# Performance work log

Measured on AMD Instinct MI355X. Metric: run time of the kernel, lower is better.

## Reference

```python
import jax, jax.numpy as jnp
import numpy as np

QMIN, QMAX = -128, 127  # get_quantized_range(8)


def setup_inputs() -> dict:
    key = jax.random.key(0)
    k1, k2, k3, k4 = jax.random.split(key, 4)
    N, IN, OUT = 8192, 4096, 4096
    x = jax.random.randint(k1, (N, IN), QMIN, QMAX + 1, dtype=jnp.int32).astype(jnp.int8)
    weight = jax.random.randint(k2, (OUT, IN), QMIN, QMAX + 1, dtype=jnp.int32).astype(jnp.int8)
    bias = jax.random.randint(k3, (OUT,), -1000, 1000, dtype=jnp.int32)
    weight_scale = jax.random.uniform(k4, (OUT,), dtype=jnp.float32, minval=1e-3, maxval=2e-2)
    return {
        "x": x,
        "weight": weight,
        "bias": bias,
        "weight_scale": weight_scale,
        "input_scale": 0.05,
        "output_scale": 0.1,
        "output_zero_point": -3,
    }


def reference(x, weight, bias, weight_scale, input_scale, output_scale, output_zero_point):
    # int8 GEMM accumulated in int32 (matches CPU path of the torch code)
    acc = jnp.matmul(x.astype(jnp.int32), weight.astype(jnp.int32).T) + bias[None, :]
    # fused per-channel dequant/requant epilogue
    scale = (input_scale * weight_scale / output_scale)[None, :]  # [1, OUT]
    out = acc.astype(jnp.float32) * scale + output_zero_point
    out = jnp.clip(jnp.round(out), QMIN, QMAX).astype(jnp.int8)
    return out
```

## Files before the change

### kernel.cpp

```cpp
#include <hip/hip_runtime.h>
#include <stdint.h>
#include <stddef.h>

typedef int v4i __attribute__((ext_vector_type(4)));

#define GLOAD16(gp, lp) __builtin_amdgcn_global_load_lds( \
    (const __attribute__((address_space(1))) void*)(gp),  \
    (__attribute__((address_space(3))) void*)(lp), 16, 0, 0)

#define PH_BAR()     __builtin_amdgcn_s_barrier()
#define WAIT_VM(n)   asm volatile("s_waitcnt vmcnt(" #n ")" ::: "memory")
#define WAIT_LGKM0() asm volatile("s_waitcnt lgkmcnt(0)" ::: "memory")
#define SCHED_FENCE() __builtin_amdgcn_sched_barrier(0)
#define PRIO1() __builtin_amdgcn_s_setprio(1)
#define PRIO0() __builtin_amdgcn_s_setprio(0)

static __device__ __forceinline__ int pack4(int a, int b, int c, int d) {
    return (a & 255) | ((b & 255) << 8) | ((c & 255) << 16) | (d << 24);
}

__global__ __launch_bounds__(256) void pack2_kernel(const int* __restrict__ srcA, v4i* __restrict__ dstA, int nA,
                                                    const int* __restrict__ srcB, v4i* __restrict__ dstB, int nB) {
    int i = blockIdx.x * blockDim.x + threadIdx.x;
    const int* src; v4i* dst;
    if (i < nA) { src = srcA; dst = dstA; }
    else { i -= nA; if (i >= nB) return; src = srcB; dst = dstB; }
    const v4i* s = reinterpret_cast<const v4i*>(src) + (size_t)i * 4;
    v4i v0 = s[0], v1 = s[1], v2 = s[2], v3 = s[3];
    v4i r;
    r.x = pack4(v0.x, v0.y, v0.z, v0.w);
    r.y = pack4(v1.x, v1.y, v1.z, v1.w);
    r.z = pack4(v2.x, v2.y, v2.z, v2.w);
    r.w = pack4(v3.x, v3.y, v3.z, v3.w);
    dst[i] = r;
}

__global__ __launch_bounds__(512, 1) void gemm_q8_mp(
    const char* __restrict__ Apk, const char* __restrict__ Bpk,
    const int* __restrict__ bias, const float* __restrict__ wscale,
    const float* __restrict__ is_p, const float* __restrict__ os_p,
    const int* __restrict__ zp_p,
    int* __restrict__ out, int K, int Ncols)
{
    __shared__ char lds[163840];

    const int tid  = threadIdx.x;
    const int wid  = tid >> 6;
    const int lane = tid & 63;
    const int l7 = lane & 7, l3 = lane >> 3;
    const int lo16 = lane & 15, hi = lane >> 4;

    int swz;
    {
        const int nwg = gridDim.x;
        const int q = nwg >> 3, r = nwg & 7;
        const int xcd = blockIdx.x & 7;
        const int base = (xcd < r) ? xcd * (q + 1) : r * (q + 1) + (xcd - r) * q;
        swz = base + (blockIdx.x >> 3);
    }
    const int nbc  = Ncols >> 8;
    const int brow = swz / nbc, bcol = swz % nbc;

    const int wr = wid >> 2, wc = wid & 3;

    const char* Ab = Apk + (size_t)(brow * 256 + wid * 8 + l3) * K + ((l7 ^ l3) << 4);
    const char* Bb = Bpk + (size_t)(bcol * 256 + wid * 8 + l3) * K + ((l7 ^ l3) << 4);

    const int colsw0 = (hi ^ l7) << 4;
    const int colsw1 = colsw0 ^ 64;
    const int aBase = (wr << 14) + (lo16 << 7);
    const int bBase = (wc << 13) + (lo16 << 7);

    v4i acc[8][4];
#pragma unroll
    for (int m = 0; m < 8; ++m)
#pragma unroll
        for (int n = 0; n < 4; ++n)
            acc[m][n] = (v4i){0, 0, 0, 0};

    v4i afA[2][2], afB[2][2], bf[4][2];

    auto stage = [&](const char* gb, int ldsOff, int h, int t) {
        const char* g = gb + (size_t)(h * 128) * K + ((size_t)t << 7);
        char* l = lds + (ldsOff + (h << 14) + (wid << 10));
        GLOAD16(g, l);
        GLOAD16(g + (size_t)64 * K, l + 8192);
    };
    auto ldAf = [&](v4i (&dst)[2][2], int bufo, int pair) {
#pragma unroll
        for (int m = 0; m < 2; ++m) {
            const int base = bufo + aBase + (pair << 12) + (m << 11);
            dst[m][0] = *(const v4i*)(lds + base + colsw0);
            dst[m][1] = *(const v4i*)(lds + base + colsw1);
        }
    };
    auto ldBf = [&](int bufo) {
#pragma unroll
        for (int n = 0; n < 4; ++n)
            bf[n][0] = *(const v4i*)(lds + 65536 + bufo + bBase + (n << 11) + colsw0);
#pragma unroll
        for (int n = 0; n < 4; ++n)
            bf[n][1] = *(const v4i*)(lds + 65536 + bufo + bBase + (n << 11) + colsw1);
    };

#define MQ(afX, p) do {                                                           \
    _Pragma("unroll") for (int s_ = 0; s_ < 2; ++s_)                              \
    _Pragma("unroll") for (int m_ = 0; m_ < 2; ++m_)                              \
    _Pragma("unroll") for (int n_ = 0; n_ < 4; ++n_)                              \
        acc[((p) << 1) + m_][n_] = __builtin_amdgcn_mfma_i32_16x16x64_i8(         \
            afX[m_][s_], bf[n_][s_], acc[((p) << 1) + m_][n_], 0, 0, 0);          \
} while (0)

    stage(Ab, 0,             0, 0);  stage(Ab, 0,             1, 0);
    stage(Bb, 65536,         0, 0);  stage(Bb, 65536,         1, 0);
    stage(Bb, 65536 + 32768, 0, 1);  stage(Bb, 65536 + 32768, 1, 1);
    WAIT_VM(4);
    PH_BAR();
    SCHED_FENCE();
    ldAf(afA, 0, 0);

    const int nt = K >> 7;
    int bcur = 0;
    for (int t = 0; t < nt - 2; ++t) {
        const int bA  = (t & 1) << 15;
        const int nbA = (~t & 1) << 15;
        int bst = bcur + 65536; if (bst >= 98304) bst -= 98304;

        ldBf(bcur);
        ldAf(afB, bA, 1);
        stage(Ab, nbA, 0, t + 1);  stage(Ab, nbA, 1, t + 1);
        PRIO1(); MQ(afA, 0); PRIO0();
        ldAf(afA, bA, 2);
        stage(Bb, 65536 + bst, 0, t + 2);  stage(Bb, 65536 + bst, 1, t + 2);
        PRIO1(); MQ(afB, 1); PRIO0();
        ldAf(afB, bA, 3);
        PRIO1(); MQ(afA, 2); PRIO0();
        WAIT_VM(4);
        WAIT_LGKM0();
        PH_BAR();
        SCHED_FENCE();
        ldAf(afA, nbA, 0);
        PRIO1(); MQ(afB, 3); PRIO0();

        bcur += 32768; if (bcur >= 98304) bcur -= 98304;
    }

    {
        const int t = nt - 2;
        const int bA  = (t & 1) << 15;
        const int nbA = (~t & 1) << 15;
        ldBf(bcur);
        ldAf(afB, bA, 1);
        stage(Ab, nbA, 0, t + 1);  stage(Ab, nbA, 1, t + 1);
        PRIO1(); MQ(afA, 0); PRIO0();
        ldAf(afA, bA, 2);
        PRIO1(); MQ(afB, 1); PRIO0();
        ldAf(afB, bA, 3);
        PRIO1(); MQ(afA, 2); PRIO0();
        WAIT_VM(0);
        WAIT_LGKM0();
        PH_BAR();
        SCHED_FENCE();
        ldAf(afA, nbA, 0);
        PRIO1(); MQ(afB, 3); PRIO0();
        bcur += 32768; if (bcur >= 98304) bcur -= 98304;
    }
    {
        const int bA = ((nt - 1) & 1) << 15;
        ldBf(bcur);
        ldAf(afB, bA, 1);
        PRIO1(); MQ(afA, 0); PRIO0();
        ldAf(afA, bA, 2);
        PRIO1(); MQ(afB, 1); PRIO0();
        ldAf(afB, bA, 3);
        PRIO1(); MQ(afA, 2); PRIO0();
        PRIO1(); MQ(afB, 3); PRIO0();
    }
#undef MQ

    const float is = *is_p, os = *os_p;
    const float zp = (float)(*zp_p);
    const int colb = (bcol << 8) + (wc << 6) + lo16;
    float sc[4]; int bv[4];
#pragma unroll
    for (int n = 0; n < 4; ++n) {
        sc[n] = is * wscale[colb + (n << 4)] / os;
        bv[n] = bias[colb + (n << 4)];
    }
#pragma unroll
    for (int m = 0; m < 8; ++m) {
#pragma unroll
        for (int j = 0; j < 4; ++j) {
            const int row = (brow << 8) + (wr << 7) + (m << 4) + (hi << 2) + j;
            int* op = out + (size_t)row * Ncols + colb;
#pragma unroll
            for (int n = 0; n < 4; ++n) {
                float f = (float)(acc[m][n][j] + bv[n]) * sc[n] + zp;
                f = rintf(f);
                f = fminf(fmaxf(f, -128.f), 127.f);
                op[n << 4] = (int)f;
            }
        }
    }
}

template <bool PACKED>
__global__ __launch_bounds__(256) void gemm_q8(
    const void* __restrict__ Ain, const void* __restrict__ Bin,
    const int* __restrict__ bias, const float* __restrict__ wscale,
    const float* __restrict__ is_p, const float* __restrict__ os_p,
    const int* __restrict__ zp_p,
    int* __restrict__ out, int Nrows, int K, int Ncols)
{
    __shared__ char Al[128 * 64];
    __shared__ char Bl[128 * 64];

    const int tid  = threadIdx.x;
    const int wid  = tid >> 6;
    const int lane = tid & 63;

    const int nbc = Ncols / 128;
    int swz = blockIdx.x;
    if ((gridDim.x & 7) == 0) {
        const int cpx = gridDim.x >> 3;
        swz = (blockIdx.x & 7) * cpx + (blockIdx.x >> 3);
    }
    const int brow = swz / nbc;
    const int bcol = swz % nbc;
    const int wr = wid >> 1, wc = wid & 1;

    v4i acc[4][4];
#pragma unroll
    for (int m = 0; m < 4; ++m)
#pragma unroll
        for (int n = 0; n < 4; ++n)
            acc[m][n] = (v4i){0, 0, 0, 0};

    const char* Ag = nullptr;
    const char* Bg = nullptr;
    if (PACKED) {
        Ag = (const char*)Ain + (size_t)(brow * 128 + wid * 32 + (lane >> 2)) * K + (lane & 3) * 16;
        Bg = (const char*)Bin + (size_t)(bcol * 128 + wid * 32 + (lane >> 2)) * K + (lane & 3) * 16;
    }
    char* aldst = Al + wid * 2048;
    char* bldst = Bl + wid * 2048;

    const int lo16 = lane & 15, hi = lane >> 4;
    const int aoff0 = (wr * 64 + lo16) * 64 + hi * 16;
    const int boff0 = (wc * 64 + lo16) * 64 + hi * 16;

    for (int k0 = 0; k0 < K; k0 += 64) {
        if (PACKED) {
            GLOAD16(Ag + k0,          aldst);
            GLOAD16(Ag + 16 * K + k0, aldst + 1024);
            GLOAD16(Bg + k0,          bldst);
            GLOAD16(Bg + 16 * K + k0, bldst + 1024);
        } else {
            const int row = tid >> 1, half = tid & 1;
            const int* sA = (const int*)Ain + (size_t)(brow * 128 + row) * K + k0 + half * 32;
            const int* sB = (const int*)Bin + (size_t)(bcol * 128 + row) * K + k0 + half * 32;
            int pa[8], pb[8];
#pragma unroll
            for (int j = 0; j < 8; ++j) {
                v4i va = reinterpret_cast<const v4i*>(sA)[j];
                v4i vb = reinterpret_cast<const v4i*>(sB)[j];
                pa[j] = pack4(va.x, va.y, va.z, va.w);
                pb[j] = pack4(vb.x, vb.y, vb.z, vb.w);
            }
            v4i* da = (v4i*)&Al[row * 64 + half * 32];
            da[0] = (v4i){pa[0], pa[1], pa[2], pa[3]};
            da[1] = (v4i){pa[4], pa[5], pa[6], pa[7]};
            v4i* db = (v4i*)&Bl[row * 64 + half * 32];
            db[0] = (v4i){pb[0], pb[1], pb[2], pb[3]};
            db[1] = (v4i){pb[4], pb[5], pb[6], pb[7]};
        }
        __syncthreads();

        v4i afr[4], bfr[4];
#pragma unroll
        for (int m = 0; m < 4; ++m)
            afr[m] = *(const v4i*)&Al[aoff0 + m * 16 * 64];
#pragma unroll
        for (int n = 0; n < 4; ++n)
            bfr[n] = *(const v4i*)&Bl[boff0 + n * 16 * 64];
#pragma unroll
        for (int m = 0; m < 4; ++m)
#pragma unroll
            for (int n = 0; n < 4; ++n)
                acc[m][n] = __builtin_amdgcn_mfma_i32_16x16x64_i8(afr[m], bfr[n], acc[m][n], 0, 0, 0);

        __syncthreads();
    }

    const float is = *is_p;
    const float os = *os_p;
    const float zp = (float)(*zp_p);
#pragma unroll
    for (int n = 0; n < 4; ++n) {
        const int col = bcol * 128 + wc * 64 + n * 16 + lo16;
        const float sc = is * wscale[col] / os;
        const int   bv = bias[col];
#pragma unroll
        for (int m = 0; m < 4; ++m) {
            const int row0 = brow * 128 + wr * 64 + m * 16 + hi * 4;
#pragma unroll
            for (int j = 0; j < 4; ++j) {
                float f = (float)(acc[m][n][j] + bv) * sc + zp;
                f = rintf(f);
                f = fminf(fmaxf(f, -128.f), 127.f);
                out[(size_t)(row0 + j) * Ncols + col] = (int)f;
            }
        }
    }
}

extern "C" void kernel_launch(void* const* d_in, const int* in_sizes, int n_in,
                              void* d_out, int out_size, void* d_ws, size_t ws_size,
                              hipStream_t stream) {
    const int*   x32    = (const int*)d_in[0];
    const int*   w32    = (const int*)d_in[1];
    const int*   bias   = (const int*)d_in[2];
    const float* wscale = (const float*)d_in[3];
    const float* isp    = (const float*)d_in[4];
    const float* osp    = (const float*)d_in[5];
    const int*   zpp    = (const int*)d_in[6];
    int* out = (int*)d_out;

    const int OUT = in_sizes[2];
    const int K   = in_sizes[1] / OUT;
    const int Nr  = in_sizes[0] / K;

    const size_t need = (size_t)Nr * K + (size_t)OUT * K;

    if (ws_size >= need) {
        char* xpk = (char*)d_ws;
        char* wpk = xpk + (size_t)Nr * K;
        const int nx16 = (Nr * K) / 16;
        const int nw16 = (OUT * K) / 16;
        pack2_kernel<<<(nx16 + nw16 + 255) / 256, 256, 0, stream>>>(
            x32, (v4i*)xpk, nx16, w32, (v4i*)wpk, nw16);
        if ((Nr & 255) == 0 && (OUT & 255) == 0 && (K & 127) == 0 && (K >> 7) >= 3) {
            const int grid8 = (Nr / 256) * (OUT / 256);
            gemm_q8_mp<<<grid8, 512, 0, stream>>>(xpk, wpk, bias, wscale, isp, osp, zpp,
                                                  out, K, OUT);
        } else {
            const int grid = (Nr / 128) * (OUT / 128);
            gemm_q8<true><<<grid, 256, 0, stream>>>(xpk, wpk, bias, wscale, isp, osp, zpp,
                                                    out, Nr, K, OUT);
        }
    } else {
        const int grid = (Nr / 128) * (OUT / 128);
        gemm_q8<false><<<grid, 256, 0, stream>>>(x32, w32, bias, wscale, isp, osp, zpp,
                                                 out, Nr, K, OUT);
    }
}
```

Baseline: 169.8 us.

## Split MFMA main loop into finer k-half phases to interleave LDS reads

Restructures the inner loop so each 128-wide k tile is processed as two 64-wide k halves. A and B fragments are loaded in smaller pieces (2 A vectors and half of B per phase) and interleaved between 8-MFMA groups, and the global-to-LDS stage calls are spread across more phases. The first B half of the next tile is prefetched after the barrier. The goal is to cut fragment register pressure and hide LDS latency better behind MFMAs. The cost is more A fragment reloads from LDS, since each A pair is now read twice per tile, and more scheduling points.

Result: no change. 172.0 us (+1.3%).

```diff
diff --git a/kernel.cpp b/kernel.cpp
--- a/kernel.cpp
+++ b/kernel.cpp
@@ -78,7 +78,7 @@
         for (int n = 0; n < 4; ++n)
             acc[m][n] = (v4i){0, 0, 0, 0};
 
-    v4i afA[2][2], afB[2][2], bf[4][2];
+    v4i afA[2], afB[2], bf[4][2];
 
     auto stage = [&](const char* gb, int ldsOff, int h, int t) {
         const char* g = gb + (size_t)(h * 128) * K + ((size_t)t << 7);
@@ -86,29 +86,23 @@
         GLOAD16(g, l);
         GLOAD16(g + (size_t)64 * K, l + 8192);
     };
-    auto ldAf = [&](v4i (&dst)[2][2], int bufo, int pair) {
-#pragma unroll
-        for (int m = 0; m < 2; ++m) {
-            const int base = bufo + aBase + (pair << 12) + (m << 11);
-            dst[m][0] = *(const v4i*)(lds + base + colsw0);
-            dst[m][1] = *(const v4i*)(lds + base + colsw1);
-        }
+    auto ldAf2 = [&](v4i (&dst)[2], int bufo, int pair, int csw) {
+#pragma unroll
+        for (int m = 0; m < 2; ++m)
+            dst[m] = *(const v4i*)(lds + bufo + aBase + (pair << 12) + (m << 11) + csw);
     };
-    auto ldBf = [&](int bufo) {
-#pragma unroll
-        for (int n = 0; n < 4; ++n)
-            bf[n][0] = *(const v4i*)(lds + 65536 + bufo + bBase + (n << 11) + colsw0);
-#pragma unroll
-        for (int n = 0; n < 4; ++n)
-            bf[n][1] = *(const v4i*)(lds + 65536 + bufo + bBase + (n << 11) + colsw1);
+    auto ldBfH = [&](int bufo, int nh, int s, int csw) {
+#pragma unroll
+        for (int k = 0; k < 2; ++k)
+            bf[(nh << 1) + k][s] =
+                *(const v4i*)(lds + 65536 + bufo + bBase + ((((nh << 1) + k)) << 11) + csw);
     };
 
-#define MQ(afX, p) do {                                                           \
-    _Pragma("unroll") for (int s_ = 0; s_ < 2; ++s_)                              \
+#define MQ8(afX, p, s) do {                                                       \
     _Pragma("unroll") for (int m_ = 0; m_ < 2; ++m_)                              \
     _Pragma("unroll") for (int n_ = 0; n_ < 4; ++n_)                              \
         acc[((p) << 1) + m_][n_] = __builtin_amdgcn_mfma_i32_16x16x64_i8(         \
-            afX[m_][s_], bf[n_][s_], acc[((p) << 1) + m_][n_], 0, 0, 0);          \
+            afX[m_], bf[n_][(s)], acc[((p) << 1) + m_][n_], 0, 0, 0);             \
 } while (0)
 
     stage(Ab, 0,             0, 0);  stage(Ab, 0,             1, 0);
@@ -117,66 +111,102 @@
     WAIT_VM(4);
     PH_BAR();
     SCHED_FENCE();
-    ldAf(afA, 0, 0);
+    ldBfH(0, 0, 0, colsw0);  ldBfH(0, 1, 0, colsw0);
+    ldAf2(afA, 0, 0, colsw0);
 
     const int nt = K >> 7;
     int bcur = 0;
     for (int t = 0; t < nt - 2; ++t) {
         const int bA  = (t & 1) << 15;
         const int nbA = (~t & 1) << 15;
-        int bst = bcur + 65536; if (bst >= 98304) bst -= 98304;
-
-        ldBf(bcur);
-        ldAf(afB, bA, 1);
-        stage(Ab, nbA, 0, t + 1);  stage(Ab, nbA, 1, t + 1);
-        PRIO1(); MQ(afA, 0); PRIO0();
-        ldAf(afA, bA, 2);
-        stage(Bb, 65536 + bst, 0, t + 2);  stage(Bb, 65536 + bst, 1, t + 2);
-        PRIO1(); MQ(afB, 1); PRIO0();
-        ldAf(afB, bA, 3);
-        PRIO1(); MQ(afA, 2); PRIO0();
+        int bnx = bcur + 32768; if (bnx >= 98304) bnx -= 98304;
+        int bst = bnx  + 32768; if (bst >= 98304) bst -= 98304;
+
+        ldAf2(afB, bA, 1, colsw0);
+        ldBfH(bcur, 0, 1, colsw1);
+        stage(Ab, nbA, 0, t + 1);
+        PRIO1(); MQ8(afA, 0, 0); PRIO0();
+        ldAf2(afA, bA, 2, colsw0);
+        ldBfH(bcur, 1, 1, colsw1);
+        stage(Ab, nbA, 1, t + 1);
+        PRIO1(); MQ8(afB, 1, 0); PRIO0();
+        ldAf2(afB, bA, 3, colsw0);
+        stage(Bb, 65536 + bst, 0, t + 2);
+        PRIO1(); MQ8(afA, 2, 0); PRIO0();
+        ldAf2(afA, bA, 0, colsw1);
+        stage(Bb, 65536 + bst, 1, t + 2);
+        PRIO1(); MQ8(afB, 3, 0); PRIO0();
+        ldAf2(afB, bA, 1, colsw1);
+        PRIO1(); MQ8(afA, 0, 1); PRIO0();
+        ldAf2(afA, bA, 2, colsw1);
+        PRIO1(); MQ8(afB, 1, 1); PRIO0();
+        ldAf2(afB, bA, 3, colsw1);
+        PRIO1(); MQ8(afA, 2, 1); PRIO0();
         WAIT_VM(4);
         WAIT_LGKM0();
         PH_BAR();
         SCHED_FENCE();
-        ldAf(afA, nbA, 0);
-        PRIO1(); MQ(afB, 3); PRIO0();
-
-        bcur += 32768; if (bcur >= 98304) bcur -= 98304;
+        ldBfH(bnx, 0, 0, colsw0);  ldBfH(bnx, 1, 0, colsw0);
+        ldAf2(afA, nbA, 0, colsw0);
+        PRIO1(); MQ8(afB, 3, 1); PRIO0();
+
+        bcur = bnx;
     }
 
     {
         const int t = nt - 2;
         const int bA  = (t & 1) << 15;
         const int nbA = (~t & 1) << 15;
-        ldBf(bcur);
-        ldAf(afB, bA, 1);
-        stage(Ab, nbA, 0, t + 1);  stage(Ab, nbA, 1, t + 1);
-        PRIO1(); MQ(afA, 0); PRIO0();
-        ldAf(afA, bA, 2);
-        PRIO1(); MQ(afB, 1); PRIO0();
-        ldAf(afB, bA, 3);
-        PRIO1(); MQ(afA, 2); PRIO0();
+        int bnx = bcur + 32768; if (bnx >= 98304) bnx -= 98304;
+
+        ldAf2(afB, bA, 1, colsw0);
+        ldBfH(bcur, 0, 1, colsw1);
+        stage(Ab, nbA, 0, t + 1);
+        PRIO1(); MQ8(afA, 0, 0); PRIO0();
+        ldAf2(afA, bA, 2, colsw0);
+        ldBfH(bcur, 1, 1, colsw1);
+        stage(Ab, nbA, 1, t + 1);
+        PRIO1(); MQ8(afB, 1, 0); PRIO0();
+        ldAf2(afB, bA, 3, colsw0);
+        PRIO1(); MQ8(afA, 2, 0); PRIO0();
+        ldAf2(afA, bA, 0, colsw1);
+        PRIO1(); MQ8(afB, 3, 0); PRIO0();
+        ldAf2(afB, bA, 1, colsw1);
+        PRIO1(); MQ8(afA, 0, 1); PRIO0();
+        ldAf2(afA, bA, 2, colsw1);
+        PRIO1(); MQ8(afB, 1, 1); PRIO0();
+        ldAf2(afB, bA, 3, colsw1);
+        PRIO1(); MQ8(afA, 2, 1); PRIO0();
         WAIT_VM(0);
         WAIT_LGKM0();
         PH_BAR();
         SCHED_FENCE();
-        ldAf(afA, nbA, 0);
-        PRIO1(); MQ(afB, 3); PRIO0();
-        bcur += 32768; if (bcur >= 98304) bcur -= 98304;
+        ldBfH(bnx, 0, 0, colsw0);  ldBfH(bnx, 1, 0, colsw0);
+        ldAf2(afA, nbA, 0, colsw0);
+        PRIO1(); MQ8(afB, 3, 1); PRIO0();
+        bcur = bnx;
     }
     {
         const int bA = ((nt - 1) & 1) << 15;
-        ldBf(bcur);
-        ldAf(afB, bA, 1);
-        PRIO1(); MQ(afA, 0); PRIO0();
-        ldAf(afA, bA, 2);
-        PRIO1(); MQ(afB, 1); PRIO0();
-        ldAf(afB, bA, 3);
-        PRIO1(); MQ(afA, 2); PRIO0();
-        PRIO1(); MQ(afB, 3); PRIO0();
-    }
-#undef MQ
+        ldAf2(afB, bA, 1, colsw0);
+        ldBfH(bcur, 0, 1, colsw1);
+        PRIO1(); MQ8(afA, 0, 0); PRIO0();
+        ldAf2(afA, bA, 2, colsw0);
+        ldBfH(bcur, 1, 1, colsw1);
+        PRIO1(); MQ8(afB, 1, 0); PRIO0();
+        ldAf2(afB, bA, 3, colsw0);
+        PRIO1(); MQ8(afA, 2, 0); PRIO0();
+        ldAf2(afA, bA, 0, colsw1);
+        PRIO1(); MQ8(afB, 3, 0); PRIO0();
+        ldAf2(afB, bA, 1, colsw1);
+        PRIO1(); MQ8(afA, 0, 1); PRIO0();
+        ldAf2(afA, bA, 2, colsw1);
+        PRIO1(); MQ8(afB, 1, 1); PRIO0();
+        ldAf2(afB, bA, 3, colsw1);
+        PRIO1(); MQ8(afA, 2, 1); PRIO0();
+        PRIO1(); MQ8(afB, 3, 1); PRIO0();
+    }
+#undef MQ8
 
     const float is = *is_p, os = *os_p;
     const float zp = (float)(*zp_p);
```

## Switch int8 GEMM main loop from 16x16x64 to 32x32x32 MFMA tiles

Applied to the files above, without the earlier changes.

Replaces the 16x16x64 int8 MFMA inner kernel with the 32x32x32 variant, with 4x2 accumulator tiles of 16 ints per wave. The LDS fragment loads are reorganised per k-substep (A and B loaded together), the B-buffer rotation is adjusted, and the epilogue is remapped to the 32x32 output layout. The aim is fewer LDS fragment reads per FLOP and fewer MFMA issues, in exchange for a different LDS access pattern that may hit bank conflicts and a changed instruction schedule.

Result: slower. 189.9 us (+11.8%).

```diff
diff --git a/kernel.cpp b/kernel.cpp
--- a/kernel.cpp
+++ b/kernel.cpp
@@ -2,7 +2,8 @@
 #include <stdint.h>
 #include <stddef.h>
 
-typedef int v4i __attribute__((ext_vector_type(4)));
+typedef int v4i  __attribute__((ext_vector_type(4)));
+typedef int v16i __attribute__((ext_vector_type(16)));
 
 #define GLOAD16(gp, lp) __builtin_amdgcn_global_load_lds( \
     (const __attribute__((address_space(1))) void*)(gp),  \
@@ -48,7 +49,7 @@
     const int wid  = tid >> 6;
     const int lane = tid & 63;
     const int l7 = lane & 7, l3 = lane >> 3;
-    const int lo16 = lane & 15, hi = lane >> 4;
+    const int l31 = lane & 31, hi5 = lane >> 5;
 
     int swz;
     {
@@ -66,19 +67,22 @@
     const char* Ab = Apk + (size_t)(brow * 256 + wid * 8 + l3) * K + ((l7 ^ l3) << 4);
     const char* Bb = Bpk + (size_t)(bcol * 256 + wid * 8 + l3) * K + ((l7 ^ l3) << 4);
 
-    const int colsw0 = (hi ^ l7) << 4;
-    const int colsw1 = colsw0 ^ 64;
-    const int aBase = (wr << 14) + (lo16 << 7);
-    const int bBase = (wc << 13) + (lo16 << 7);
-
-    v4i acc[8][4];
-#pragma unroll
-    for (int m = 0; m < 8; ++m)
-#pragma unroll
-        for (int n = 0; n < 4; ++n)
-            acc[m][n] = (v4i){0, 0, 0, 0};
-
-    v4i afA[2][2], afB[2][2], bf[4][2];
+    int colw[4];
+#pragma unroll
+    for (int s = 0; s < 4; ++s) colw[s] = (((s << 1) + hi5) ^ l7) << 4;
+    const int aBase = (wr << 14) + (l31 << 7);
+    const int bBase = (wc << 13) + (l31 << 7);
+
+    v16i acc[4][2];
+#pragma unroll
+    for (int m = 0; m < 4; ++m)
+#pragma unroll
+        for (int n = 0; n < 2; ++n)
+#pragma unroll
+            for (int j = 0; j < 16; ++j)
+                acc[m][n][j] = 0;
+
+    v4i afA[4], afB[4], bfA[2], bfB[2];
 
     auto stage = [&](const char* gb, int ldsOff, int h, int t) {
         const char* g = gb + (size_t)(h * 128) * K + ((size_t)t << 7);
@@ -86,29 +90,22 @@
         GLOAD16(g, l);
         GLOAD16(g + (size_t)64 * K, l + 8192);
     };
-    auto ldAf = [&](v4i (&dst)[2][2], int bufo, int pair) {
-#pragma unroll
-        for (int m = 0; m < 2; ++m) {
-            const int base = bufo + aBase + (pair << 12) + (m << 11);
-            dst[m][0] = *(const v4i*)(lds + base + colsw0);
-            dst[m][1] = *(const v4i*)(lds + base + colsw1);
-        }
+    auto ldAs = [&](v4i (&dst)[4], int bufo, int s) {
+#pragma unroll
+        for (int m = 0; m < 4; ++m)
+            dst[m] = *(const v4i*)(lds + bufo + aBase + (m << 12) + colw[s]);
     };
-    auto ldBf = [&](int bufo) {
-#pragma unroll
-        for (int n = 0; n < 4; ++n)
-            bf[n][0] = *(const v4i*)(lds + 65536 + bufo + bBase + (n << 11) + colsw0);
-#pragma unroll
-        for (int n = 0; n < 4; ++n)
-            bf[n][1] = *(const v4i*)(lds + 65536 + bufo + bBase + (n << 11) + colsw1);
+    auto ldBs = [&](v4i (&dst)[2], int bufo, int s) {
+#pragma unroll
+        for (int n = 0; n < 2; ++n)
+            dst[n] = *(const v4i*)(lds + 65536 + bufo + bBase + (n << 12) + colw[s]);
     };
 
-#define MQ(afX, p) do {                                                           \
-    _Pragma("unroll") for (int s_ = 0; s_ < 2; ++s_)                              \
-    _Pragma("unroll") for (int m_ = 0; m_ < 2; ++m_)                              \
-    _Pragma("unroll") for (int n_ = 0; n_ < 4; ++n_)                              \
-        acc[((p) << 1) + m_][n_] = __builtin_amdgcn_mfma_i32_16x16x64_i8(         \
-            afX[m_][s_], bf[n_][s_], acc[((p) << 1) + m_][n_], 0, 0, 0);          \
+#define MQ32(afX, bfX) do {                                                       \
+    _Pragma("unroll") for (int m_ = 0; m_ < 4; ++m_)                              \
+    _Pragma("unroll") for (int n_ = 0; n_ < 2; ++n_)                              \
+        acc[m_][n_] = __builtin_amdgcn_mfma_i32_32x32x32_i8(                      \
+            afX[m_], bfX[n_], acc[m_][n_], 0, 0, 0);                              \
 } while (0)
 
     stage(Ab, 0,             0, 0);  stage(Ab, 0,             1, 0);
@@ -117,88 +114,93 @@
     WAIT_VM(4);
     PH_BAR();
     SCHED_FENCE();
-    ldAf(afA, 0, 0);
+    ldAs(afA, 0, 0);
+    ldBs(bfA, 0, 0);
 
     const int nt = K >> 7;
     int bcur = 0;
     for (int t = 0; t < nt - 2; ++t) {
         const int bA  = (t & 1) << 15;
         const int nbA = (~t & 1) << 15;
-        int bst = bcur + 65536; if (bst >= 98304) bst -= 98304;
-
-        ldBf(bcur);
-        ldAf(afB, bA, 1);
+        int bnx = bcur + 32768; if (bnx >= 98304) bnx -= 98304;
+        int bst = bnx  + 32768; if (bst >= 98304) bst -= 98304;
+
+        ldAs(afB, bA, 1);  ldBs(bfB, bcur, 1);
         stage(Ab, nbA, 0, t + 1);  stage(Ab, nbA, 1, t + 1);
-        PRIO1(); MQ(afA, 0); PRIO0();
-        ldAf(afA, bA, 2);
+        PRIO1(); MQ32(afA, bfA); PRIO0();
+        ldAs(afA, bA, 2);  ldBs(bfA, bcur, 2);
         stage(Bb, 65536 + bst, 0, t + 2);  stage(Bb, 65536 + bst, 1, t + 2);
-        PRIO1(); MQ(afB, 1); PRIO0();
-        ldAf(afB, bA, 3);
-        PRIO1(); MQ(afA, 2); PRIO0();
+        PRIO1(); MQ32(afB, bfB); PRIO0();
+        ldAs(afB, bA, 3);  ldBs(bfB, bcur, 3);
+        PRIO1(); MQ32(afA, bfA); PRIO0();
         WAIT_VM(4);
         WAIT_LGKM0();
         PH_BAR();
         SCHED_FENCE();
-        ldAf(afA, nbA, 0);
-        PRIO1(); MQ(afB, 3); PRIO0();
-
-        bcur += 32768; if (bcur >= 98304) bcur -= 98304;
+        ldAs(afA, nbA, 0);  ldBs(bfA, bnx, 0);
+        PRIO1(); MQ32(afB, bfB); PRIO0();
+
+        bcur = bnx;
     }
 
     {
         const int t = nt - 2;
         const int bA  = (t & 1) << 15;
         const int nbA = (~t & 1) << 15;
-        ldBf(bcur);
-        ldAf(afB, bA, 1);
+        int bnx = bcur + 32768; if (bnx >= 98304) bnx -= 98304;
+
+        ldAs(afB, bA, 1);  ldBs(bfB, bcur, 1);
         stage(Ab, nbA, 0, t + 1);  stage(Ab, nbA, 1, t + 1);
-        PRIO1(); MQ(afA, 0); PRIO0();
-        ldAf(afA, bA, 2);
-        PRIO1(); MQ(afB, 1); PRIO0();
-        ldAf(afB, bA, 3);
-        PRIO1(); MQ(afA, 2); PRIO0();
+        PRIO1(); MQ32(afA, bfA); PRIO0();
+        ldAs(afA, bA, 2);  ldBs(bfA, bcur, 2);
+        PRIO1(); MQ32(afB, bfB); PRIO0();
+        ldAs(afB, bA, 3);  ldBs(bfB, bcur, 3);
+        PRIO1(); MQ32(afA, bfA); PRIO0();
         WAIT_VM(0);
         WAIT_LGKM0();
         PH_BAR();
         SCHED_FENCE();
-        ldAf(afA, nbA, 0);
-        PRIO1(); MQ(afB, 3); PRIO0();
-        bcur += 32768; if (bcur >= 98304) bcur -= 98304;
+        ldAs(afA, nbA, 0);  ldBs(bfA, bnx, 0);
+        PRIO1(); MQ32(afB, bfB); PRIO0();
+        bcur = bnx;
     }
     {
         const int bA = ((nt - 1) & 1) << 15;
-        ldBf(bcur);
-        ldAf(afB, bA, 1);
-        PRIO1(); MQ(afA, 0); PRIO0();
-        ldAf(afA, bA, 2);
-        PRIO1(); MQ(afB, 1); PRIO0();
-        ldAf(afB, bA, 3);
-        PRIO1(); MQ(afA, 2); PRIO0();
-        PRIO1(); MQ(afB, 3); PRIO0();
-    }
-#undef MQ
+        ldAs(afB, bA, 1);  ldBs(bfB, bcur, 1);
+        PRIO1(); MQ32(afA, bfA); PRIO0();
+        ldAs(afA, bA, 2);  ldBs(bfA, bcur, 2);
+        PRIO1(); MQ32(afB, bfB); PRIO0();
+        ldAs(afB, bA, 3);  ldBs(bfB, bcur, 3);
+        PRIO1(); MQ32(afA, bfA); PRIO0();
+        PRIO1(); MQ32(afB, bfB); PRIO0();
+    }
+#undef MQ32
 
     const float is = *is_p, os = *os_p;
     const float zp = (float)(*zp_p);
-    const int colb = (bcol << 8) + (wc << 6) + lo16;
-    float sc[4]; int bv[4];
-#pragma unroll
-    for (int n = 0; n < 4; ++n) {
-        sc[n] = is * wscale[colb + (n << 4)] / os;
-        bv[n] = bias[colb + (n << 4)];
-    }
-#pragma unroll
-    for (int m = 0; m < 8; ++m) {
-#pragma unroll
-        for (int j = 0; j < 4; ++j) {
-            const int row = (brow << 8) + (wr << 7) + (m << 4) + (hi << 2) + j;
-            int* op = out + (size_t)row * Ncols + colb;
-#pragma unroll
-            for (int n = 0; n < 4; ++n) {
-                float f = (float)(acc[m][n][j] + bv[n]) * sc[n] + zp;
-                f = rintf(f);
-                f = fminf(fmaxf(f, -128.f), 127.f);
-                op[n << 4] = (int)f;
+    const int colb = (bcol << 8) + (wc << 6) + l31;
+    float sc[2]; int bv[2];
+#pragma unroll
+    for (int n = 0; n < 2; ++n) {
+        sc[n] = is * wscale[colb + (n << 5)] / os;
+        bv[n] = bias[colb + (n << 5)];
+    }
+#pragma unroll
+    for (int mf = 0; mf < 4; ++mf) {
+        const int rowbase = (brow << 8) + (wr << 7) + (mf << 5) + (hi5 << 2);
+#pragma unroll
+        for (int rg = 0; rg < 4; ++rg) {
+#pragma unroll
+            for (int j = 0; j < 4; ++j) {
+                const int row = rowbase + (rg << 3) + j;
+                int* op = out + (size_t)row * Ncols + colb;
+#pragma unroll
+                for (int n = 0; n < 2; ++n) {
+                    float f = (float)(acc[mf][n][(rg << 2) + j] + bv[n]) * sc[n] + zp;
+                    f = rintf(f);
+                    f = fminf(fmaxf(f, -128.f), 127.f);
+                    op[n << 5] = (int)f;
+                }
             }
         }
     }
```
